# Performance work log

Hardware: AMD Instinct MI355X
Metric: run time of the kernel (lower is better)

Reference implementation:

```python
import jax, jax.numpy as jnp
import numpy as np

N, Q, K, H, C = 32, 1, 2048, 16, 64
E = H * C  # 1024
N_ACT = 2


def setup_inputs() -> dict:
    key = jax.random.key(0)
    ks = jax.random.split(key, 8)
    q = jax.random.normal(ks[0], (N, Q, E), dtype=jnp.float32)
    k = jax.random.normal(ks[1], (N, K, H, C), dtype=jnp.float32)
    v = jax.random.normal(ks[2], (N, K, H, C), dtype=jnp.float32)
    m = jnp.ones((N, K), dtype=bool)
    s_in = 1.0 / np.sqrt(E)
    W_in = jax.random.uniform(ks[3], (N_ACT * E, E), jnp.float32, -s_in, s_in)
    b_in = jax.random.uniform(ks[4], (N_ACT * E,), jnp.float32, -s_in, s_in)
    W_out = jax.random.uniform(ks[5], (E, E), jnp.float32, -s_in, s_in)
    b_out = jax.random.uniform(ks[6], (E,), jnp.float32, -s_in, s_in)
    return {"q": q, "k": k, "v": v, "m": m, "W_in": W_in, "b_in": b_in,
            "W_out": W_out, "b_out": b_out}


def reference(q, k, v, m, W_in, b_in, W_out, b_out):
    norm = jnp.sqrt(jnp.asarray(C, q.dtype))
    # in_proj then split into per-branch queries: [N,Q,H,C] each
    qp = (q @ W_in.T + b_in).reshape(N, Q, H, N_ACT * C)
    q_smax, q_coda = qp[..., :C], qp[..., C:]
    mexp = m[:, None, :, None]  # [N,1,K,1]

    # branch 1: masked softmax over keys
    aff_s = jnp.einsum('nqhc,nkhc->nqkh', q_smax / norm, k)
    aff_s = jnp.where(mexp, aff_s, -jnp.inf)
    aff_s = jax.nn.softmax(aff_s, axis=-2)

    # branch 2: compositional de-attention (tanh affinity * sigmoid gate)
    aff_c = jnp.tanh(jnp.einsum('nqhc,nkhc->nqkh', q_coda / norm, k))
    gate = -jnp.abs(q_coda[:, :, None] - k[:, None]).sum(-1) / norm  # [N,Q,K,H]
    gate = 2.0 * jax.nn.sigmoid(gate) * mexp.astype(q.dtype)
    aff_c = aff_c * gate

    aff = (aff_s + aff_c) / N_ACT
    mix = jnp.einsum('nqkh,nkhc->nqhc', aff, v)  # [N,Q,H,C]
    return mix.reshape(N, Q, E) @ W_out.T + b_out
```

## Files before the change

kernel.cpp:

```cpp
#include <hip/hip_runtime.h>

#define NB 32
#define KK 2048
#define HH 16
#define CC 64
#define EE 1024
#define RIN 2048
#define HC 1024
#define CHUNK 64
#define NCH (KK / CHUNK)

__device__ __forceinline__ float dot4(const float4 a, const float4 b) {
    return fmaf(a.x, b.x, fmaf(a.y, b.y, fmaf(a.z, b.z, a.w * b.w)));
}

__device__ __forceinline__ float rcp_fast(float x) {
    return __builtin_amdgcn_rcpf(x);
}

__device__ __forceinline__ float tanh_fast(float x) {
    x = fminf(fmaxf(x, -15.0f), 15.0f);
    float t = __expf(2.0f * x);
    return (t - 1.0f) * rcp_fast(t + 1.0f);
}

__device__ __forceinline__ float gate_fn(float a) {
    return 2.0f * rcp_fast(1.0f + __expf(a));
}

__device__ __forceinline__ void gload_lds16(const float* g, float* l) {
    __builtin_amdgcn_global_load_lds(
        (const __attribute__((address_space(1))) void*)g,
        (__attribute__((address_space(3))) void*)l,
        16, 0, 0);
}

__global__ __launch_bounds__(256) void gemv_batched(
        const float* __restrict__ X,
        const float* __restrict__ W,
        const float* __restrict__ b,
        float* __restrict__ Y,
        int ystride) {
    const int tid  = threadIdx.x;
    const int lane = tid & 63;
    const int w    = tid >> 6;
    const int r    = blockIdx.x * 4 + w;
    const float* Wr = W + (size_t)r * EE;

    float acc[NB];
#pragma unroll
    for (int n = 0; n < NB; ++n) acc[n] = 0.0f;

#pragma unroll
    for (int ch = 0; ch < EE; ch += 256) {
        const float4 wv = *(const float4*)(Wr + ch + lane * 4);
#pragma unroll
        for (int n = 0; n < NB; ++n) {
            const float4 xv = *(const float4*)(X + n * EE + ch + lane * 4);
            acc[n] = fmaf(wv.x, xv.x, acc[n]);
            acc[n] = fmaf(wv.y, xv.y, acc[n]);
            acc[n] = fmaf(wv.z, xv.z, acc[n]);
            acc[n] = fmaf(wv.w, xv.w, acc[n]);
        }
    }
#pragma unroll
    for (int n = 0; n < NB; ++n) {
#pragma unroll
        for (int m = 32; m >= 1; m >>= 1)
            acc[n] += __shfl_xor(acc[n], m);
    }
    if (lane == 0) {
        const float bb = b[r];
#pragma unroll
        for (int n = 0; n < NB; ++n)
            Y[n * ystride + r] = acc[n] + bb;
    }
}

#define ABLK 512
__global__ __launch_bounds__(ABLK, 4) void attn_kernel(
        const float* __restrict__ Kp,
        const float* __restrict__ Vp,
        const float* __restrict__ qp,
        float* __restrict__ mix) {
    __shared__ float buf[2][CHUNK][CC];
    __shared__ float w_s[KK];
    __shared__ float w_c[KK];
    float* red = &buf[1][0][0];
    float (*mr)[CC] = (float(*)[CC])&buf[0][0][0];

    const int tid  = threadIdx.x;
    const int lane = tid & 63;
    const int w    = tid >> 6;
    const int c8   = tid & 7;
    const int rloc = (tid >> 3) & 63;
    const int n    = blockIdx.x >> 4;
    const int h    = blockIdx.x & 15;

    const float* qrow = qp + n * RIN + h * (2 * CC) + c8 * 8;
    const float4 qsa = *(const float4*)(qrow);
    const float4 qsb = *(const float4*)(qrow + 4);
    const float4 qca = *(const float4*)(qrow + CC);
    const float4 qcb = *(const float4*)(qrow + CC + 4);

    const size_t base = (size_t)n * KK * HC + h * CC;
    const float* kb = Kp + base;
    const float* vb = Vp + base;

    const size_t g_lane_off = (size_t)(lane >> 4) * HC + (lane & 15) * 4;

#define STAGE(gbase, c, bsel)                                                  \
    {                                                                          \
        const float* g0 = (gbase) + (size_t)((c) * CHUNK + w * 8) * HC + g_lane_off; \
        gload_lds16(g0,                &buf[(bsel)][w * 8][0]);                \
        gload_lds16(g0 + 4 * (size_t)HC, &buf[(bsel)][w * 8 + 4][0]);          \
    }

    STAGE(kb, 0, 0);
    __syncthreads();
    int cur = 0;
    for (int c = 0; c < NCH; ++c) {
        if (c + 1 < NCH) STAGE(kb, c + 1, cur ^ 1);

        const float* rp = &buf[cur][rloc][c8 * 8];
        const float4 ka = *(const float4*)(rp);
        const float4 kb4 = *(const float4*)(rp + 4);
        float ds = dot4(qsa, ka) + dot4(qsb, kb4);
        float dc = dot4(qca, ka) + dot4(qcb, kb4);
        float ga = fabsf(qca.x - ka.x) + fabsf(qca.y - ka.y)
                 + fabsf(qca.z - ka.z) + fabsf(qca.w - ka.w)
                 + fabsf(qcb.x - kb4.x) + fabsf(qcb.y - kb4.y)
                 + fabsf(qcb.z - kb4.z) + fabsf(qcb.w - kb4.w);
#pragma unroll
        for (int m = 1; m <= 4; m <<= 1) {
            ds += __shfl_xor(ds, m);
            dc += __shfl_xor(dc, m);
            ga += __shfl_xor(ga, m);
        }
        const int grow = c * CHUNK + rloc;
        if (c8 == 0)      w_s[grow] = ds * 0.125f;
        else if (c8 == 1) w_c[grow] = tanh_fast(dc * 0.125f) * gate_fn(ga * 0.125f);

        __syncthreads();
        cur ^= 1;
    }

    STAGE(vb, 0, 0);

    float lm = -1e30f;
#pragma unroll
    for (int i = 0; i < KK / ABLK; ++i) lm = fmaxf(lm, w_s[tid + i * ABLK]);
#pragma unroll
    for (int m = 1; m <= 32; m <<= 1) lm = fmaxf(lm, __shfl_xor(lm, m));
    if (lane == 0) red[w] = lm;
    __syncthreads();
    float gm = red[0];
#pragma unroll
    for (int ww = 1; ww < ABLK / 64; ++ww) gm = fmaxf(gm, red[ww]);

    float lsum = 0.0f;
#pragma unroll
    for (int i = 0; i < KK / ABLK; ++i) {
        const float e = __expf(w_s[tid + i * ABLK] - gm);
        w_s[tid + i * ABLK] = e;
        lsum += e;
    }
#pragma unroll
    for (int m = 1; m <= 32; m <<= 1) lsum += __shfl_xor(lsum, m);
    __syncthreads();
    if (lane == 0) red[w] = lsum;
    __syncthreads();
    float tot = 0.0f;
#pragma unroll
    for (int ww = 0; ww < ABLK / 64; ++ww) tot += red[ww];
    const float invl = 0.5f / tot;

#pragma unroll
    for (int i = 0; i < KK / ABLK; ++i) {
        const int idx = tid + i * ABLK;
        w_s[idx] = fmaf(w_s[idx], invl, 0.5f * w_c[idx]);
    }
    __syncthreads();

    const int col = tid & 63;
    float acc = 0.0f;
    cur = 0;
    for (int c = 0; c < NCH; ++c) {
        if (c + 1 < NCH) STAGE(vb, c + 1, cur ^ 1);
#pragma unroll
        for (int i = 0; i < 8; ++i) {
            const int row = w * 8 + i;
            acc = fmaf(w_s[c * CHUNK + row], buf[cur][row][col], acc);
        }
        __syncthreads();
        cur ^= 1;
    }

    mr[w][col] = acc;
    __syncthreads();
    if (tid < CC) {
        float s = 0.0f;
#pragma unroll
        for (int ww = 0; ww < ABLK / 64; ++ww) s += mr[ww][tid];
        mix[n * EE + h * CC + tid] = s;
    }
#undef STAGE
}

extern "C" void kernel_launch(void* const* d_in, const int* in_sizes, int n_in,
                              void* d_out, int out_size, void* d_ws, size_t ws_size,
                              hipStream_t stream) {
    const float* q     = (const float*)d_in[0];
    const float* k     = (const float*)d_in[1];
    const float* v     = (const float*)d_in[2];
    const float* W_in  = (const float*)d_in[4];
    const float* b_in  = (const float*)d_in[5];
    const float* W_out = (const float*)d_in[6];
    const float* b_out = (const float*)d_in[7];
    float* out = (float*)d_out;

    float* qp  = (float*)d_ws;
    float* mix = qp + NB * RIN;

    gemv_batched<<<RIN / 4, 256, 0, stream>>>(q, W_in, b_in, qp, RIN);
    attn_kernel<<<NB * HH, ABLK, 0, stream>>>(k, v, qp, mix);
    gemv_batched<<<EE / 4, 256, 0, stream>>>(mix, W_out, b_out, out, EE);
}
```

Before: 162.4 us.

## Deepen attention K/V staging to a 4-slot ring with vmcnt-based waits

Replaces the double-buffered LDS staging of K and V chunks with a 4-slot ring that keeps three chunk loads in flight. Full __syncthreads are swapped for explicit s_waitcnt vmcnt/lgkmcnt plus s_barrier, so each step waits only for its own chunk. The aim is to hide more global-memory latency in this bandwidth-bound attention pass. In exchange, LDS use doubles for the staging buffer, which may lower occupancy, and the hand-tuned waitcnt counts must stay correct for the barrier logic to hold.

```diff
diff --git a/kernel.cpp b/kernel.cpp
--- a/kernel.cpp
+++ b/kernel.cpp
@@ -83,10 +83,10 @@
         const float* __restrict__ Vp,
         const float* __restrict__ qp,
         float* __restrict__ mix) {
-    __shared__ float buf[2][CHUNK][CC];
+    __shared__ float buf[4][CHUNK][CC];
     __shared__ float w_s[KK];
     __shared__ float w_c[KK];
-    float* red = &buf[1][0][0];
+    float* red = &buf[3][0][0];
     float (*mr)[CC] = (float(*)[CC])&buf[0][0][0];
 
     const int tid  = threadIdx.x;
@@ -94,6 +94,7 @@
     const int w    = tid >> 6;
     const int c8   = tid & 7;
     const int rloc = (tid >> 3) & 63;
+    const int col  = lane;
     const int n    = blockIdx.x >> 4;
     const int h    = blockIdx.x & 15;
 
@@ -109,43 +110,75 @@
 
     const size_t g_lane_off = (size_t)(lane >> 4) * HC + (lane & 15) * 4;
 
-#define STAGE(gbase, c, bsel)                                                  \
-    {                                                                          \
+#define STAGE(gbase, c, slot)                                                   \
+    {                                                                           \
         const float* g0 = (gbase) + (size_t)((c) * CHUNK + w * 8) * HC + g_lane_off; \
-        gload_lds16(g0,                &buf[(bsel)][w * 8][0]);                \
-        gload_lds16(g0 + 4 * (size_t)HC, &buf[(bsel)][w * 8 + 4][0]);          \
-    }
-
-    STAGE(kb, 0, 0);
-    __syncthreads();
-    int cur = 0;
-    for (int c = 0; c < NCH; ++c) {
-        if (c + 1 < NCH) STAGE(kb, c + 1, cur ^ 1);
-
-        const float* rp = &buf[cur][rloc][c8 * 8];
-        const float4 ka = *(const float4*)(rp);
-        const float4 kb4 = *(const float4*)(rp + 4);
-        float ds = dot4(qsa, ka) + dot4(qsb, kb4);
-        float dc = dot4(qca, ka) + dot4(qcb, kb4);
-        float ga = fabsf(qca.x - ka.x) + fabsf(qca.y - ka.y)
-                 + fabsf(qca.z - ka.z) + fabsf(qca.w - ka.w)
-                 + fabsf(qcb.x - kb4.x) + fabsf(qcb.y - kb4.y)
-                 + fabsf(qcb.z - kb4.z) + fabsf(qcb.w - kb4.w);
-#pragma unroll
-        for (int m = 1; m <= 4; m <<= 1) {
-            ds += __shfl_xor(ds, m);
-            dc += __shfl_xor(dc, m);
-            ga += __shfl_xor(ga, m);
-        }
-        const int grow = c * CHUNK + rloc;
-        if (c8 == 0)      w_s[grow] = ds * 0.125f;
-        else if (c8 == 1) w_c[grow] = tanh_fast(dc * 0.125f) * gate_fn(ga * 0.125f);
-
-        __syncthreads();
-        cur ^= 1;
-    }
-
-    STAGE(vb, 0, 0);
+        gload_lds16(g0,                  &buf[(slot)][w * 8][0]);               \
+        gload_lds16(g0 + 4 * (size_t)HC, &buf[(slot)][w * 8 + 4][0]);           \
+    }
+
+#define WAITBAR(c)                                                              \
+    {                                                                           \
+        if ((c) <= NCH - 3)      asm volatile("s_waitcnt vmcnt(4)" ::: "memory"); \
+        else if ((c) == NCH - 2) asm volatile("s_waitcnt vmcnt(2)" ::: "memory"); \
+        else                     asm volatile("s_waitcnt vmcnt(0)" ::: "memory"); \
+        __builtin_amdgcn_s_barrier();                                           \
+        __builtin_amdgcn_sched_barrier(0);                                      \
+    }
+
+#define BAR_LGKM()                                                              \
+    {                                                                           \
+        asm volatile("s_waitcnt lgkmcnt(0)" ::: "memory");                      \
+        __builtin_amdgcn_s_barrier();                                           \
+        __builtin_amdgcn_sched_barrier(0);                                      \
+    }
+
+#define COMPK(c, slot)                                                          \
+    {                                                                           \
+        const float* rp = &buf[(slot)][rloc][c8 * 8];                           \
+        const float4 ka = *(const float4*)(rp);                                 \
+        const float4 kx = *(const float4*)(rp + 4);                             \
+        float ds = dot4(qsa, ka) + dot4(qsb, kx);                               \
+        float dc = dot4(qca, ka) + dot4(qcb, kx);                               \
+        float ga = fabsf(qca.x - ka.x) + fabsf(qca.y - ka.y)                    \
+                 + fabsf(qca.z - ka.z) + fabsf(qca.w - ka.w)                    \
+                 + fabsf(qcb.x - kx.x) + fabsf(qcb.y - kx.y)                    \
+                 + fabsf(qcb.z - kx.z) + fabsf(qcb.w - kx.w);                   \
+        ds += __shfl_xor(ds, 1); ds += __shfl_xor(ds, 2); ds += __shfl_xor(ds, 4); \
+        dc += __shfl_xor(dc, 1); dc += __shfl_xor(dc, 2); dc += __shfl_xor(dc, 4); \
+        ga += __shfl_xor(ga, 1); ga += __shfl_xor(ga, 2); ga += __shfl_xor(ga, 4); \
+        const int grow = (c) * CHUNK + rloc;                                    \
+        if (c8 == 0)      w_s[grow] = ds * 0.125f;                              \
+        else if (c8 == 1) w_c[grow] = tanh_fast(dc * 0.125f) * gate_fn(ga * 0.125f); \
+    }
+
+#define COMPV(c, slot)                                                          \
+    {                                                                           \
+        _Pragma("unroll")                                                       \
+        for (int i = 0; i < 8; ++i) {                                           \
+            const int row = w * 8 + i;                                          \
+            acc = fmaf(w_s[(c) * CHUNK + row], buf[(slot)][row][col], acc);     \
+        }                                                                       \
+    }
+
+    STAGE(kb, 0, 0); STAGE(kb, 1, 1); STAGE(kb, 2, 2);
+    for (int cc = 0; cc < NCH; cc += 4) {
+        WAITBAR(cc + 0);
+        STAGE(kb, cc + 3, 3);
+        COMPK(cc + 0, 0);
+        WAITBAR(cc + 1);
+        if (cc + 4 < NCH) STAGE(kb, cc + 4, 0);
+        COMPK(cc + 1, 1);
+        WAITBAR(cc + 2);
+        if (cc + 5 < NCH) STAGE(kb, cc + 5, 1);
+        COMPK(cc + 2, 2);
+        WAITBAR(cc + 3);
+        if (cc + 6 < NCH) STAGE(kb, cc + 6, 2);
+        COMPK(cc + 3, 3);
+    }
+    BAR_LGKM();
+
+    STAGE(vb, 0, 0); STAGE(vb, 1, 1); STAGE(vb, 2, 2);
 
     float lm = -1e30f;
 #pragma unroll
@@ -153,7 +186,7 @@
 #pragma unroll
     for (int m = 1; m <= 32; m <<= 1) lm = fmaxf(lm, __shfl_xor(lm, m));
     if (lane == 0) red[w] = lm;
-    __syncthreads();
+    BAR_LGKM();
     float gm = red[0];
 #pragma unroll
     for (int ww = 1; ww < ABLK / 64; ++ww) gm = fmaxf(gm, red[ww]);
@@ -167,9 +200,9 @@
     }
 #pragma unroll
     for (int m = 1; m <= 32; m <<= 1) lsum += __shfl_xor(lsum, m);
-    __syncthreads();
+    BAR_LGKM();
     if (lane == 0) red[w] = lsum;
-    __syncthreads();
+    BAR_LGKM();
     float tot = 0.0f;
 #pragma unroll
     for (int ww = 0; ww < ABLK / 64; ++ww) tot += red[ww];
@@ -180,24 +213,26 @@
         const int idx = tid + i * ABLK;
         w_s[idx] = fmaf(w_s[idx], invl, 0.5f * w_c[idx]);
     }
-    __syncthreads();
-
-    const int col = tid & 63;
+    BAR_LGKM();
+
     float acc = 0.0f;
-    cur = 0;
-    for (int c = 0; c < NCH; ++c) {
-        if (c + 1 < NCH) STAGE(vb, c + 1, cur ^ 1);
-#pragma unroll
-        for (int i = 0; i < 8; ++i) {
-            const int row = w * 8 + i;
-            acc = fmaf(w_s[c * CHUNK + row], buf[cur][row][col], acc);
-        }
-        __syncthreads();
-        cur ^= 1;
-    }
-
+    for (int cc = 0; cc < NCH; cc += 4) {
+        WAITBAR(cc + 0);
+        STAGE(vb, cc + 3, 3);
+        COMPV(cc + 0, 0);
+        WAITBAR(cc + 1);
+        if (cc + 4 < NCH) STAGE(vb, cc + 4, 0);
+        COMPV(cc + 1, 1);
+        WAITBAR(cc + 2);
+        if (cc + 5 < NCH) STAGE(vb, cc + 5, 1);
+        COMPV(cc + 2, 2);
+        WAITBAR(cc + 3);
+        if (cc + 6 < NCH) STAGE(vb, cc + 6, 2);
+        COMPV(cc + 3, 3);
+    }
+    BAR_LGKM();
     mr[w][col] = acc;
-    __syncthreads();
+    BAR_LGKM();
     if (tid < CC) {
         float s = 0.0f;
 #pragma unroll
@@ -205,6 +240,10 @@
         mix[n * EE + h * CC + tid] = s;
     }
 #undef STAGE
+#undef WAITBAR
+#undef BAR_LGKM
+#undef COMPK
+#undef COMPV
 }
 
 extern "C" void kernel_launch(void* const* d_in, const int* in_sizes, int n_in,
```

Result: no change. 163.3 us (+0.5%).

## Split attention into key-segmented score, softmax, mix and reduce kernels

Applied to the files above, without the earlier changes.

Replaces the single per-(batch,head) attention kernel with four kernels: a score kernel over 32 key segments per batch covering all heads, a separate softmax kernel, a segmented weighted-V mix kernel writing partial sums, and a reduction kernel. Each key/value row of 1024 floats is now read contiguously by one block, with register prefetching instead of LDS async copies. The aim is more blocks and better coalescing for the K/V streaming, which should raise memory bandwidth use. In exchange it adds extra launches and global round-trips for scores, weights and partial sums.

```diff
diff --git a/kernel.cpp b/kernel.cpp
--- a/kernel.cpp
+++ b/kernel.cpp
@@ -7,8 +7,8 @@
 #define EE 1024
 #define RIN 2048
 #define HC 1024
-#define CHUNK 64
-#define NCH (KK / CHUNK)
+#define SEG 32
+#define RPB (KK / SEG)
 
 __device__ __forceinline__ float dot4(const float4 a, const float4 b) {
     return fmaf(a.x, b.x, fmaf(a.y, b.y, fmaf(a.z, b.z, a.w * b.w)));
@@ -26,13 +26,6 @@
 
 __device__ __forceinline__ float gate_fn(float a) {
     return 2.0f * rcp_fast(1.0f + __expf(a));
-}
-
-__device__ __forceinline__ void gload_lds16(const float* g, float* l) {
-    __builtin_amdgcn_global_load_lds(
-        (const __attribute__((address_space(1))) void*)g,
-        (__attribute__((address_space(3))) void*)l,
-        16, 0, 0);
 }
 
 __global__ __launch_bounds__(256) void gemv_batched(
@@ -77,134 +70,159 @@
     }
 }
 
-#define ABLK 512
-__global__ __launch_bounds__(ABLK, 4) void attn_kernel(
+__global__ __launch_bounds__(256) void score_kernel(
         const float* __restrict__ Kp,
-        const float* __restrict__ Vp,
         const float* __restrict__ qp,
-        float* __restrict__ mix) {
-    __shared__ float buf[2][CHUNK][CC];
-    __shared__ float w_s[KK];
-    __shared__ float w_c[KK];
-    float* red = &buf[1][0][0];
-    float (*mr)[CC] = (float(*)[CC])&buf[0][0][0];
-
-    const int tid  = threadIdx.x;
-    const int lane = tid & 63;
-    const int w    = tid >> 6;
-    const int c8   = tid & 7;
-    const int rloc = (tid >> 3) & 63;
-    const int n    = blockIdx.x >> 4;
-    const int h    = blockIdx.x & 15;
-
-    const float* qrow = qp + n * RIN + h * (2 * CC) + c8 * 8;
-    const float4 qsa = *(const float4*)(qrow);
-    const float4 qsb = *(const float4*)(qrow + 4);
-    const float4 qca = *(const float4*)(qrow + CC);
-    const float4 qcb = *(const float4*)(qrow + CC + 4);
-
-    const size_t base = (size_t)n * KK * HC + h * CC;
-    const float* kb = Kp + base;
-    const float* vb = Vp + base;
-
-    const size_t g_lane_off = (size_t)(lane >> 4) * HC + (lane & 15) * 4;
-
-#define STAGE(gbase, c, bsel)                                                  \
-    {                                                                          \
-        const float* g0 = (gbase) + (size_t)((c) * CHUNK + w * 8) * HC + g_lane_off; \
-        gload_lds16(g0,                &buf[(bsel)][w * 8][0]);                \
-        gload_lds16(g0 + 4 * (size_t)HC, &buf[(bsel)][w * 8 + 4][0]);          \
-    }
-
-    STAGE(kb, 0, 0);
-    __syncthreads();
-    int cur = 0;
-    for (int c = 0; c < NCH; ++c) {
-        if (c + 1 < NCH) STAGE(kb, c + 1, cur ^ 1);
-
-        const float* rp = &buf[cur][rloc][c8 * 8];
-        const float4 ka = *(const float4*)(rp);
-        const float4 kb4 = *(const float4*)(rp + 4);
-        float ds = dot4(qsa, ka) + dot4(qsb, kb4);
-        float dc = dot4(qca, ka) + dot4(qcb, kb4);
-        float ga = fabsf(qca.x - ka.x) + fabsf(qca.y - ka.y)
-                 + fabsf(qca.z - ka.z) + fabsf(qca.w - ka.w)
-                 + fabsf(qcb.x - kb4.x) + fabsf(qcb.y - kb4.y)
-                 + fabsf(qcb.z - kb4.z) + fabsf(qcb.w - kb4.w);
-#pragma unroll
-        for (int m = 1; m <= 4; m <<= 1) {
-            ds += __shfl_xor(ds, m);
-            dc += __shfl_xor(dc, m);
-            ga += __shfl_xor(ga, m);
-        }
-        const int grow = c * CHUNK + rloc;
-        if (c8 == 0)      w_s[grow] = ds * 0.125f;
-        else if (c8 == 1) w_c[grow] = tanh_fast(dc * 0.125f) * gate_fn(ga * 0.125f);
-
-        __syncthreads();
-        cur ^= 1;
-    }
-
-    STAGE(vb, 0, 0);
-
+        float* __restrict__ ws_s,
+        float* __restrict__ ws_c) {
+    const int t    = threadIdx.x;
+    const int h    = t >> 4;
+    const int c16  = t & 15;
+    const int n    = blockIdx.x >> 5;
+    const int seg  = blockIdx.x & 31;
+    const int row0 = seg * RPB;
+
+    const float* qb = qp + n * RIN + h * (2 * CC) + c16 * 4;
+    const float4 qs = *(const float4*)(qb);
+    const float4 qc = *(const float4*)(qb + CC);
+
+    const float* kb = Kp + ((size_t)(n * KK + row0)) * HC + h * CC + c16 * 4;
+    float* so = ws_s + (size_t)(n * HH + h) * KK + row0;
+    float* co = ws_c + (size_t)(n * HH + h) * KK + row0;
+
+#define PROC(r, kv)                                                             \
+    {                                                                           \
+        float ds = dot4(qs, kv);                                                \
+        float dc = dot4(qc, kv);                                                \
+        float ga = fabsf(qc.x - kv.x) + fabsf(qc.y - kv.y)                      \
+                 + fabsf(qc.z - kv.z) + fabsf(qc.w - kv.w);                     \
+        ds += __shfl_xor(ds, 1); ds += __shfl_xor(ds, 2);                       \
+        ds += __shfl_xor(ds, 4); ds += __shfl_xor(ds, 8);                       \
+        dc += __shfl_xor(dc, 1); dc += __shfl_xor(dc, 2);                       \
+        dc += __shfl_xor(dc, 4); dc += __shfl_xor(dc, 8);                       \
+        ga += __shfl_xor(ga, 1); ga += __shfl_xor(ga, 2);                       \
+        ga += __shfl_xor(ga, 4); ga += __shfl_xor(ga, 8);                       \
+        if (c16 == 0)      so[(r)] = ds * 0.125f;                               \
+        else if (c16 == 1) co[(r)] = tanh_fast(dc * 0.125f) * gate_fn(ga * 0.125f); \
+    }
+
+    float4 b0 = *(const float4*)(kb + (size_t)0 * HC);
+    float4 b1 = *(const float4*)(kb + (size_t)1 * HC);
+    float4 b2 = *(const float4*)(kb + (size_t)2 * HC);
+    float4 b3 = *(const float4*)(kb + (size_t)3 * HC);
+    for (int r = 0; r < RPB; r += 4) {
+        const int pn = (r + 4 < RPB) ? r + 4 : r;
+        const float4 n0 = *(const float4*)(kb + (size_t)(pn + 0) * HC);
+        const float4 n1 = *(const float4*)(kb + (size_t)(pn + 1) * HC);
+        const float4 n2 = *(const float4*)(kb + (size_t)(pn + 2) * HC);
+        const float4 n3 = *(const float4*)(kb + (size_t)(pn + 3) * HC);
+        PROC(r + 0, b0); PROC(r + 1, b1); PROC(r + 2, b2); PROC(r + 3, b3);
+        b0 = n0; b1 = n1; b2 = n2; b3 = n3;
+    }
+#undef PROC
+}
+
+__global__ __launch_bounds__(256) void softmax_kernel(
+        const float* __restrict__ ws_s,
+        const float* __restrict__ ws_c,
+        float* __restrict__ wq) {
+    __shared__ float red[4];
+    const int t    = threadIdx.x;
+    const int lane = t & 63;
+    const int w    = t >> 6;
+    const size_t base = (size_t)blockIdx.x * KK;
+
+    float sv[8];
     float lm = -1e30f;
 #pragma unroll
-    for (int i = 0; i < KK / ABLK; ++i) lm = fmaxf(lm, w_s[tid + i * ABLK]);
+    for (int i = 0; i < 8; ++i) {
+        sv[i] = ws_s[base + t + i * 256];
+        lm = fmaxf(lm, sv[i]);
+    }
 #pragma unroll
     for (int m = 1; m <= 32; m <<= 1) lm = fmaxf(lm, __shfl_xor(lm, m));
     if (lane == 0) red[w] = lm;
     __syncthreads();
-    float gm = red[0];
-#pragma unroll
-    for (int ww = 1; ww < ABLK / 64; ++ww) gm = fmaxf(gm, red[ww]);
-
-    float lsum = 0.0f;
-#pragma unroll
-    for (int i = 0; i < KK / ABLK; ++i) {
-        const float e = __expf(w_s[tid + i * ABLK] - gm);
-        w_s[tid + i * ABLK] = e;
-        lsum += e;
-    }
-#pragma unroll
-    for (int m = 1; m <= 32; m <<= 1) lsum += __shfl_xor(lsum, m);
-    __syncthreads();
-    if (lane == 0) red[w] = lsum;
-    __syncthreads();
-    float tot = 0.0f;
-#pragma unroll
-    for (int ww = 0; ww < ABLK / 64; ++ww) tot += red[ww];
+    const float gm = fmaxf(fmaxf(red[0], red[1]), fmaxf(red[2], red[3]));
+
+    float ls = 0.0f;
+#pragma unroll
+    for (int i = 0; i < 8; ++i) {
+        sv[i] = __expf(sv[i] - gm);
+        ls += sv[i];
+    }
+#pragma unroll
+    for (int m = 1; m <= 32; m <<= 1) ls += __shfl_xor(ls, m);
+    __syncthreads();
+    if (lane == 0) red[w] = ls;
+    __syncthreads();
+    const float tot = red[0] + red[1] + red[2] + red[3];
     const float invl = 0.5f / tot;
-
-#pragma unroll
-    for (int i = 0; i < KK / ABLK; ++i) {
-        const int idx = tid + i * ABLK;
-        w_s[idx] = fmaf(w_s[idx], invl, 0.5f * w_c[idx]);
-    }
-    __syncthreads();
-
-    const int col = tid & 63;
+#pragma unroll
+    for (int i = 0; i < 8; ++i)
+        wq[base + t + i * 256] = fmaf(sv[i], invl, 0.5f * ws_c[base + t + i * 256]);
+}
+
+__global__ __launch_bounds__(256) void mix_kernel(
+        const float* __restrict__ Vp,
+        const float* __restrict__ wq,
+        float* __restrict__ partial) {
+    __shared__ float wlds[RPB][HH];
+    const int t    = threadIdx.x;
+    const int h    = t >> 4;
+    const int c16  = t & 15;
+    const int n    = blockIdx.x >> 5;
+    const int seg  = blockIdx.x & 31;
+    const int row0 = seg * RPB;
+
+#pragma unroll
+    for (int i = 0; i < 4; ++i) {
+        const int idx = t + i * 256;
+        const int hh  = idx >> 6;
+        const int r   = idx & 63;
+        wlds[r][hh] = wq[(size_t)(n * HH + hh) * KK + row0 + r];
+    }
+    __syncthreads();
+
+    const float* vb = Vp + ((size_t)(n * KK + row0)) * HC + h * CC + c16 * 4;
+    float4 acc = make_float4(0.f, 0.f, 0.f, 0.f);
+
+    float4 b0 = *(const float4*)(vb + (size_t)0 * HC);
+    float4 b1 = *(const float4*)(vb + (size_t)1 * HC);
+    float4 b2 = *(const float4*)(vb + (size_t)2 * HC);
+    float4 b3 = *(const float4*)(vb + (size_t)3 * HC);
+    for (int r = 0; r < RPB; r += 4) {
+        const int pn = (r + 4 < RPB) ? r + 4 : r;
+        const float4 n0 = *(const float4*)(vb + (size_t)(pn + 0) * HC);
+        const float4 n1 = *(const float4*)(vb + (size_t)(pn + 1) * HC);
+        const float4 n2 = *(const float4*)(vb + (size_t)(pn + 2) * HC);
+        const float4 n3 = *(const float4*)(vb + (size_t)(pn + 3) * HC);
+        const float w0 = wlds[r + 0][h], w1 = wlds[r + 1][h];
+        const float w2 = wlds[r + 2][h], w3 = wlds[r + 3][h];
+        acc.x = fmaf(w0, b0.x, acc.x); acc.y = fmaf(w0, b0.y, acc.y);
+        acc.z = fmaf(w0, b0.z, acc.z); acc.w = fmaf(w0, b0.w, acc.w);
+        acc.x = fmaf(w1, b1.x, acc.x); acc.y = fmaf(w1, b1.y, acc.y);
+        acc.z = fmaf(w1, b1.z, acc.z); acc.w = fmaf(w1, b1.w, acc.w);
+        acc.x = fmaf(w2, b2.x, acc.x); acc.y = fmaf(w2, b2.y, acc.y);
+        acc.z = fmaf(w2, b2.z, acc.z); acc.w = fmaf(w2, b2.w, acc.w);
+        acc.x = fmaf(w3, b3.x, acc.x); acc.y = fmaf(w3, b3.y, acc.y);
+        acc.z = fmaf(w3, b3.z, acc.z); acc.w = fmaf(w3, b3.w, acc.w);
+        b0 = n0; b1 = n1; b2 = n2; b3 = n3;
+    }
+    *(float4*)(partial + (size_t)(n * SEG + seg) * EE + h * CC + c16 * 4) = acc;
+}
+
+__global__ __launch_bounds__(256) void reduce_kernel(
+        const float* __restrict__ partial,
+        float* __restrict__ mix) {
+    const int f = blockIdx.x * 256 + threadIdx.x;
+    const int n = f >> 10;
+    const int e = f & 1023;
     float acc = 0.0f;
-    cur = 0;
-    for (int c = 0; c < NCH; ++c) {
-        if (c + 1 < NCH) STAGE(vb, c + 1, cur ^ 1);
-#pragma unroll
-        for (int i = 0; i < 8; ++i) {
-            const int row = w * 8 + i;
-            acc = fmaf(w_s[c * CHUNK + row], buf[cur][row][col], acc);
-        }
-        __syncthreads();
-        cur ^= 1;
-    }
-
-    mr[w][col] = acc;
-    __syncthreads();
-    if (tid < CC) {
-        float s = 0.0f;
-#pragma unroll
-        for (int ww = 0; ww < ABLK / 64; ++ww) s += mr[ww][tid];
-        mix[n * EE + h * CC + tid] = s;
-    }
-#undef STAGE
+#pragma unroll
+    for (int s = 0; s < SEG; ++s)
+        acc += partial[(size_t)(n * SEG + s) * EE + e];
+    mix[f] = acc;
 }
 
 extern "C" void kernel_launch(void* const* d_in, const int* in_sizes, int n_in,
@@ -219,10 +237,17 @@
     const float* b_out = (const float*)d_in[7];
     float* out = (float*)d_out;
 
-    float* qp  = (float*)d_ws;
-    float* mix = qp + NB * RIN;
-
-    gemv_batched<<<RIN / 4, 256, 0, stream>>>(q, W_in, b_in, qp, RIN);
-    attn_kernel<<<NB * HH, ABLK, 0, stream>>>(k, v, qp, mix);
-    gemv_batched<<<EE / 4, 256, 0, stream>>>(mix, W_out, b_out, out, EE);
-}
+    float* qp      = (float*)d_ws;
+    float* ws_s    = qp      + NB * RIN;
+    float* ws_c    = ws_s    + NB * HH * KK;
+    float* wq      = ws_c    + NB * HH * KK;
+    float* partial = wq      + NB * HH * KK;
+    float* mix     = partial + NB * SEG * EE;
+
+    gemv_batched  <<<RIN / 4,        256, 0, stream>>>(q, W_in, b_in, qp, RIN);
+    score_kernel  <<<NB * SEG,       256, 0, stream>>>(k, qp, ws_s, ws_c);
+    softmax_kernel<<<NB * HH,        256, 0, stream>>>(ws_s, ws_c, wq);
+    mix_kernel    <<<NB * SEG,       256, 0, stream>>>(v, wq, partial);
+    reduce_kernel <<<NB * EE / 256,  256, 0, stream>>>(partial, mix);
+    gemv_batched  <<<EE / 4,         256, 0, stream>>>(mix, W_out, b_out, out, EE);
+}
```

Result: slower. 190.8 us (+17.5%).
